# Kernel optimization log

Hardware: AMD Instinct MI355X
Metric: run time of the kernel (lower is better)

Reference implementation:

```python
import jax, jax.numpy as jnp
import numpy as np

N, C, H_IN, H_PAD, P = 64, 64, 110, 112, 4


def setup_inputs() -> dict:
    key = jax.random.key(0)
    k1, k2 = jax.random.split(key)
    x = jax.random.normal(k1, (N, C, H_IN, H_IN), dtype=jnp.float32)
    # binary gating mask at padded resolution (mask values in {0,1})
    batch_mask = jax.random.bernoulli(k2, 0.5, (N, C, H_PAD, H_PAD)).astype(jnp.float32)
    return {"x": x, "batch_mask": batch_mask, "p_size": P}


def reference(x, batch_mask, p_size):
    Hin, Win = x.shape[2], x.shape[3]
    pad_s = batch_mask.shape[2] - Hin  # right/bottom zero pad, as in torch F.pad
    xp = jnp.pad(x, ((0, 0), (0, 0), (0, pad_s), (0, pad_s))) if pad_s else x
    n, c, H, W = xp.shape
    h, w = H // p_size, W // p_size
    m = xp * batch_mask
    # depthwise all-ones conv with kernel=stride=p_size == block sum-pool
    pooled = m.reshape(n, c, h, p_size, w, p_size).sum(axis=(3, 5))  # [n,c,h,w]
    b = (pooled > 0).astype(xp.dtype)
    # repeat/reshape/permute chain in the original == nearest-neighbor upsample by p_size
    b_expanded = jnp.repeat(jnp.repeat(b, p_size, axis=2), p_size, axis=3)  # [n,c,H,W]
    out = xp * b_expanded
    if pad_s:
        out = out[:, :, :Hin, :Hin]
    return out
```

## Files before the change

kernel.cpp:

```cpp
#include <hip/hip_runtime.h>


#define HIN   110
#define HPAD  112
#define PTILE 28
#define TILES (PTILE*PTILE)
#define PLANE_X (HIN*HIN)
#define PLANE_M (HPAD*HPAD)
#define NPLANES 4096
#define TOTAL_TILES (NPLANES*TILES)

__global__ __launch_bounds__(256) void spatial_gate_kernel(
    const float* __restrict__ x,
    const float* __restrict__ mask,
    float* __restrict__ out)
{
    unsigned gid = blockIdx.x * 256u + threadIdx.x;
    if (gid >= TOTAL_TILES) return;

    unsigned plane = gid / TILES;
    unsigned t     = gid - plane * TILES;
    unsigned pr    = t / PTILE;
    unsigned pc    = t - pr * PTILE;

    const float* xp = x    + (size_t)plane * PLANE_X;
    const float* mp = mask + (size_t)plane * PLANE_M;
    float*       op = out  + (size_t)plane * PLANE_X;

    const int  col0   = (int)pc * 4;
    const bool full_c = (pc < PTILE - 1);

    float xv[4][4];
    float total = 0.0f;

    #pragma unroll
    for (int r = 0; r < 4; ++r) {
        int row = (int)pr * 4 + r;
        float x0 = 0.f, x1 = 0.f, x2 = 0.f, x3 = 0.f;
        float p0 = 0.f, p1 = 0.f, p2 = 0.f, p3 = 0.f;
        if (row < HIN) {
            const float* xr = xp + row * HIN + col0;
            float2 a = *(const float2*)xr;
            x0 = a.x; x1 = a.y;
            if (full_c) {
                float2 bq = *(const float2*)(xr + 2);
                x2 = bq.x; x3 = bq.y;
            }
            float4 mv = *(const float4*)(mp + row * HPAD + col0);
            p0 = __fmul_rn(x0, mv.x);
            p1 = __fmul_rn(x1, mv.y);
            p2 = __fmul_rn(x2, mv.z);
            p3 = __fmul_rn(x3, mv.w);
        }
        float rs = __fadd_rn(__fadd_rn(__fadd_rn(p0, p1), p2), p3);
        total = __fadd_rn(total, rs);
        xv[r][0] = x0; xv[r][1] = x1; xv[r][2] = x2; xv[r][3] = x3;
    }

    const float b = (total > 0.0f) ? 1.0f : 0.0f;

    #pragma unroll
    for (int r = 0; r < 4; ++r) {
        int row = (int)pr * 4 + r;
        if (row < HIN) {
            float* orow = op + row * HIN + col0;
            float2 s0; s0.x = xv[r][0] * b; s0.y = xv[r][1] * b;
            *(float2*)orow = s0;
            if (full_c) {
                float2 s1; s1.x = xv[r][2] * b; s1.y = xv[r][3] * b;
                *(float2*)(orow + 2) = s1;
            }
        }
    }
}

extern "C" void kernel_launch(void* const* d_in, const int* in_sizes, int n_in,
                              void* d_out, int out_size, void* d_ws, size_t ws_size,
                              hipStream_t stream) {
    const float* x    = (const float*)d_in[0];
    const float* mask = (const float*)d_in[1];
    float* out = (float*)d_out;

    dim3 grid(TOTAL_TILES / 256);
    dim3 block(256);
    hipLaunchKernelGGL(spatial_gate_kernel, grid, block, 0, stream, x, mask, out);
}
```

Measured before the change: 459.6 us.

## Stage quarter-plane row bands in LDS for coalesced float4 loads and stores

Each block now handles a 28-row band of one plane. It copies x and the mask into shared memory with contiguous float4 loads, computes the 196 tile gates from LDS, then writes the output as contiguous float4 stores. This replaces the per-thread strided float2 accesses, whose stride made global memory access poorly coalesced. In exchange it adds about 25KB of LDS per block, two barriers, integer divisions in the store loop, and only 196 of 256 threads do work in the gate phase.

```diff
diff --git a/kernel.cpp b/kernel.cpp
--- a/kernel.cpp
+++ b/kernel.cpp
@@ -1,76 +1,85 @@
 #include <hip/hip_runtime.h>
 
 
-#define HIN   110
-#define HPAD  112
-#define PTILE 28
-#define TILES (PTILE*PTILE)
-#define PLANE_X (HIN*HIN)
-#define PLANE_M (HPAD*HPAD)
-#define NPLANES 4096
-#define TOTAL_TILES (NPLANES*TILES)
+#define HIN     110
+#define HPAD    112
+#define PLANE_X 12100
+#define PLANE_M 12544
+#define QROWS   28
+#define QX      (QROWS*HIN)
+#define QX4     (QX/4)
+#define QM      (QROWS*HPAD)
+#define QM4     (QM/4)
+#define NTILES  196
 
 __global__ __launch_bounds__(256) void spatial_gate_kernel(
     const float* __restrict__ x,
     const float* __restrict__ mask,
     float* __restrict__ out)
 {
-    unsigned gid = blockIdx.x * 256u + threadIdx.x;
-    if (gid >= TOTAL_TILES) return;
+    __shared__ __align__(16) float sx[QX];
+    __shared__ __align__(16) float sm[QM];
+    __shared__ float sg[NTILES];
 
-    unsigned plane = gid / TILES;
-    unsigned t     = gid - plane * TILES;
-    unsigned pr    = t / PTILE;
-    unsigned pc    = t - pr * PTILE;
+    const int tid = threadIdx.x;
+    const unsigned blk   = blockIdx.x;
+    const unsigned plane = blk >> 2;
+    const unsigned q     = blk & 3;
+    const int r0    = (int)q * QROWS;
+    const int vrows = (r0 + QROWS <= HIN) ? QROWS : (HIN - r0);
+    const int nval  = vrows * HIN;
+    const int nval4 = nval >> 2;
 
-    const float* xp = x    + (size_t)plane * PLANE_X;
-    const float* mp = mask + (size_t)plane * PLANE_M;
-    float*       op = out  + (size_t)plane * PLANE_X;
+    const float4* __restrict__ xg = (const float4*)(x    + (size_t)plane*PLANE_X + (size_t)r0*HIN);
+    const float4* __restrict__ mg = (const float4*)(mask + (size_t)plane*PLANE_M + (size_t)r0*HPAD);
+    float4*       __restrict__ og = (float4*)      (out  + (size_t)plane*PLANE_X + (size_t)r0*HIN);
+    float4* sx4 = (float4*)sx;
+    float4* sm4 = (float4*)sm;
 
-    const int  col0   = (int)pc * 4;
-    const bool full_c = (pc < PTILE - 1);
+    for (int i = tid; i < nval4; i += 256) sx4[i] = xg[i];
+    for (int i = nval4 + tid; i < QX4; i += 256) sx4[i] = make_float4(0.f,0.f,0.f,0.f);
+    for (int i = tid; i < QM4; i += 256) sm4[i] = mg[i];
+    __syncthreads();
 
-    float xv[4][4];
-    float total = 0.0f;
+    if (tid < NTILES) {
+        const int tr   = tid / 28;
+        const int tc   = tid - tr * 28;
+        const int col0 = tc * 4;
+        float total = 0.f;
+        #pragma unroll
+        for (int r = 0; r < 4; ++r) {
+            const int lr = tr * 4 + r;
+            const float* xr = sx + lr * HIN;
+            const float* mr = sm + lr * HPAD + col0;
+            float p[4];
+            #pragma unroll
+            for (int j = 0; j < 4; ++j) {
+                const int c  = col0 + j;
+                const int cs = (c < HIN) ? c : 0;
+                float xv = xr[cs];
+                xv = (c < HIN) ? xv : 0.f;
+                p[j] = __fmul_rn(xv, mr[j]);
+            }
+            const float rs = __fadd_rn(__fadd_rn(__fadd_rn(p[0], p[1]), p[2]), p[3]);
+            total = __fadd_rn(total, rs);
+        }
+        sg[tid] = (total > 0.f) ? 1.f : 0.f;
+    }
+    __syncthreads();
 
-    #pragma unroll
-    for (int r = 0; r < 4; ++r) {
-        int row = (int)pr * 4 + r;
-        float x0 = 0.f, x1 = 0.f, x2 = 0.f, x3 = 0.f;
-        float p0 = 0.f, p1 = 0.f, p2 = 0.f, p3 = 0.f;
-        if (row < HIN) {
-            const float* xr = xp + row * HIN + col0;
-            float2 a = *(const float2*)xr;
-            x0 = a.x; x1 = a.y;
-            if (full_c) {
-                float2 bq = *(const float2*)(xr + 2);
-                x2 = bq.x; x3 = bq.y;
-            }
-            float4 mv = *(const float4*)(mp + row * HPAD + col0);
-            p0 = __fmul_rn(x0, mv.x);
-            p1 = __fmul_rn(x1, mv.y);
-            p2 = __fmul_rn(x2, mv.z);
-            p3 = __fmul_rn(x3, mv.w);
+    for (int i4 = tid; i4 < nval4; i4 += 256) {
+        const float4 v = sx4[i4];
+        const int i = i4 << 2;
+        float o[4];
+        float e[4] = {v.x, v.y, v.z, v.w};
+        #pragma unroll
+        for (int j = 0; j < 4; ++j) {
+            const int idx = i + j;
+            const int row = idx / HIN;
+            const int col = idx - row * HIN;
+            o[j] = e[j] * sg[(row >> 2) * 28 + (col >> 2)];
         }
-        float rs = __fadd_rn(__fadd_rn(__fadd_rn(p0, p1), p2), p3);
-        total = __fadd_rn(total, rs);
-        xv[r][0] = x0; xv[r][1] = x1; xv[r][2] = x2; xv[r][3] = x3;
-    }
-
-    const float b = (total > 0.0f) ? 1.0f : 0.0f;
-
-    #pragma unroll
-    for (int r = 0; r < 4; ++r) {
-        int row = (int)pr * 4 + r;
-        if (row < HIN) {
-            float* orow = op + row * HIN + col0;
-            float2 s0; s0.x = xv[r][0] * b; s0.y = xv[r][1] * b;
-            *(float2*)orow = s0;
-            if (full_c) {
-                float2 s1; s1.x = xv[r][2] * b; s1.y = xv[r][3] * b;
-                *(float2*)(orow + 2) = s1;
-            }
-        }
+        og[i4] = make_float4(o[0], o[1], o[2], o[3]);
     }
 }
 
@@ -81,7 +90,7 @@
     const float* mask = (const float*)d_in[1];
     float* out = (float*)d_out;
 
-    dim3 grid(TOTAL_TILES / 256);
+    dim3 grid(4096u * 4u);
     dim3 block(256);
     hipLaunchKernelGGL(spatial_gate_kernel, grid, block, 0, stream, x, mask, out);
 }
```

After: 451.3 us. No clear change (-1.8%).
